# Kernel tuning notes

Measured on AMD Instinct MI355X. Metric: run time of the kernel, lower is better.

## Reference

```python
import jax, jax.numpy as jnp
import numpy as np

WD, WH, WW = 2, 7, 7          # window size (D, H, W)
SD, SH, SW = 1, 3, 3          # shift size
DIM, NH = 128, 4              # channels, heads
B, D, H, W = 8, 8, 56, 56     # input dims
N = WD * WH * WW              # tokens per window = 98
HIDDEN = int(DIM * 4.0)


def _rel_index_np():
    coords = np.stack(np.meshgrid(np.arange(WD), np.arange(WH), np.arange(WW), indexing='ij'))
    coords = coords.reshape(3, -1)                      # [3, N]
    rel = (coords[:, :, None] - coords[:, None, :]).transpose(1, 2, 0)  # [N, N, 3]
    rel[:, :, 0] += WD - 1
    rel[:, :, 1] += WH - 1
    rel[:, :, 2] += WW - 1
    rel[:, :, 0] *= (2 * WH - 1) * (2 * WW - 1)
    rel[:, :, 1] *= (2 * WW - 1)
    return rel.sum(-1).astype(np.int32)                 # [N, N]


def _window_partition_np(x):
    b, d, h, w, c = x.shape
    x = x.reshape(b, d // WD, WD, h // WH, WH, w // WW, WW, c)
    return x.transpose(0, 1, 3, 5, 2, 4, 6, 7).reshape(-1, N, c)


def _attn_mask_np():
    img = np.zeros((1, D, H, W, 1), np.float32)
    cnt = 0
    for ds in (slice(0, -WD), slice(-WD, -SD), slice(-SD, None)):
        for hs in (slice(0, -WH), slice(-WH, -SH), slice(-SH, None)):
            for ws in (slice(0, -WW), slice(-WW, -SW), slice(-SW, None)):
                img[:, ds, hs, ws, :] = cnt
                cnt += 1
    mw = _window_partition_np(img).reshape(-1, N)       # [nW, N]
    am = mw[:, None, :] - mw[:, :, None]
    return np.where(am != 0, -100.0, 0.0).astype(np.float32)  # [nW, N, N]


def setup_inputs() -> dict:
    key = jax.random.key(0)
    ks = jax.random.split(key, 8)
    s = 0.02
    return {
        'x': jax.random.normal(ks[0], (B, D, H, W, DIM), jnp.float32),
        'mask_matrix': jnp.asarray(_attn_mask_np()),
        'rel_index': jnp.asarray(_rel_index_np()),
        'norm1_g': jnp.ones((DIM,), jnp.float32),
        'norm1_b': jnp.zeros((DIM,), jnp.float32),
        'qkv_w': s * jax.random.normal(ks[1], (DIM, 3 * DIM), jnp.float32),
        'qkv_b': jnp.zeros((3 * DIM,), jnp.float32),
        'rpb': s * jax.random.normal(ks[2], ((2 * WD - 1) * (2 * WH - 1) * (2 * WW - 1), NH), jnp.float32),
        'proj_w': s * jax.random.normal(ks[3], (DIM, DIM), jnp.float32),
        'proj_b': jnp.zeros((DIM,), jnp.float32),
        'norm2_g': jnp.ones((DIM,), jnp.float32),
        'norm2_b': jnp.zeros((DIM,), jnp.float32),
        'fc1_w': s * jax.random.normal(ks[4], (DIM, HIDDEN), jnp.float32),
        'fc1_b': jnp.zeros((HIDDEN,), jnp.float32),
        'fc2_w': s * jax.random.normal(ks[5], (HIDDEN, DIM), jnp.float32),
        'fc2_b': jnp.zeros((DIM,), jnp.float32),
    }


def _ln(x, g, b):
    mu = jnp.mean(x, -1, keepdims=True)
    v = jnp.mean((x - mu) ** 2, -1, keepdims=True)
    return (x - mu) * jax.lax.rsqrt(v + 1e-5) * g + b


def _partition(x):
    b, d, h, w, c = x.shape
    x = x.reshape(b, d // WD, WD, h // WH, WH, w // WW, WW, c)
    return x.transpose(0, 1, 3, 5, 2, 4, 6, 7).reshape(-1, N, c)


def _reverse(win, b, d, h, w):
    c = win.shape[-1]
    x = win.reshape(b, d // WD, h // WH, w // WW, WD, WH, WW, c)
    return x.transpose(0, 1, 4, 2, 5, 3, 6, 7).reshape(b, d, h, w, c)


def _forward(x, mask_matrix, rel_index, norm1_g, norm1_b, qkv_w, qkv_b, rpb,
             proj_w, proj_b, norm2_g, norm2_b, fc1_w, fc1_b, fc2_w, fc2_b):
    b, d, h, w, c = x.shape
    shortcut = x
    y = _ln(x, norm1_g, norm1_b)
    # pad to multiples of window size (static; 0 for chosen dims)
    pd, ph, pw = (-d) % WD, (-h) % WH, (-w) % WW
    y = jnp.pad(y, ((0, 0), (0, pd), (0, ph), (0, pw), (0, 0)))
    dp, hp, wp = d + pd, h + ph, w + pw
    # cyclic shift
    y = jnp.roll(y, (-SD, -SH, -SW), axis=(1, 2, 3))
    win = _partition(y)                                   # [Bw, N, C]
    bw = win.shape[0]
    hd = c // NH
    qkv = (win @ qkv_w + qkv_b).reshape(bw, N, 3, NH, hd).transpose(2, 0, 3, 1, 4)
    q, k, v = qkv[0] * (hd ** -0.5), qkv[1], qkv[2]       # [Bw, NH, N, hd]
    attn = jnp.einsum('bhnd,bhmd->bhnm', q, k)            # [Bw, NH, N, N]
    bias = rpb[rel_index].transpose(2, 0, 1)              # [NH, N, N]
    attn = attn + bias[None]
    nw = mask_matrix.shape[0]
    attn = attn.reshape(bw // nw, nw, NH, N, N) + mask_matrix[None, :, None]
    attn = jax.nn.softmax(attn.reshape(bw, NH, N, N), axis=-1)
    o = jnp.einsum('bhnm,bhmd->bhnd', attn, v).transpose(0, 2, 1, 3).reshape(bw, N, c)
    o = o @ proj_w + proj_b
    y = _reverse(o, b, dp, hp, wp)
    y = jnp.roll(y, (SD, SH, SW), axis=(1, 2, 3))[:, :d, :h, :w, :]
    x1 = shortcut + y                                     # first residual
    z = _ln(x1, norm2_g, norm2_b)
    z = jax.nn.gelu(z @ fc1_w + fc1_b, approximate=False)
    # NOTE: source code's call() returns drop_path(mlp(norm2(x))) WITHOUT the
    # second residual add; we replicate exactly (drop_path is Identity at rate 0).
    return z @ fc2_w + fc2_b


def reference(x, mask_matrix, rel_index, norm1_g, norm1_b, qkv_w, qkv_b, rpb,
              proj_w, proj_b, norm2_g, norm2_b, fc1_w, fc1_b, fc2_w, fc2_b):
    return _forward(x, mask_matrix, rel_index, norm1_g, norm1_b, qkv_w, qkv_b,
                    rpb, proj_w, proj_b, norm2_g, norm2_b, fc1_w, fc1_b, fc2_w, fc2_b)


if __name__ == '__main__':
    out = reference(**setup_inputs())
    print(out.shape)
```

## Files before the change

### kernel.cpp

```cpp
#include <hip/hip_runtime.h>
#include <hip/hip_bf16.h>

typedef __attribute__((ext_vector_type(8))) short bf16x8;
typedef __attribute__((ext_vector_type(4))) float f32x4;

#define MFMA(a,b,c) __builtin_amdgcn_mfma_f32_16x16x32_bf16((a),(b),(c),0,0,0)
#define WAVE_LDS_FENCE() do { asm volatile("s_waitcnt lgkmcnt(0)" ::: "memory"); \
                              __builtin_amdgcn_sched_barrier(0); } while (0)

static constexpr int NTOK = 8 * 8 * 56 * 56;
static constexpr int NT   = 98;
static constexpr int NWIN = 2048;
static constexpr int NN   = NT * NT;

__device__ __forceinline__ unsigned short f2bf(float f) {
  unsigned r;
  asm("v_cvt_pk_bf16_f32 %0, %1, %1" : "=v"(r) : "v"(f));
  return (unsigned short)r;
}
__device__ __forceinline__ unsigned f2bf2(float lo, float hi) {
  unsigned r;
  asm("v_cvt_pk_bf16_f32 %0, %1, %2" : "=v"(r) : "v"(lo), "v"(hi));
  return r;
}
__device__ __forceinline__ float bf2f(unsigned short s) {
  union { unsigned u; float f; } v; v.u = ((unsigned)s) << 16; return v.f;
}
union U8 { unsigned u[4]; bf16x8 v; };

__device__ __forceinline__ size_t srow_of(int t) {
  int widx = t / NT, n = t - widx * NT;
  int bb = widx >> 8, wb = widx & 255;
  int dW = wb >> 6, hW = (wb >> 3) & 7, wW = wb & 7;
  int dr = n / 49, rem = n - dr * 49, hr = rem / 7, wr = rem - hr * 7;
  int dsh = (dW * 2 + dr + 1) & 7;
  int hs = hW * 7 + hr + 3; if (hs >= 56) hs -= 56;
  int wsv = wW * 7 + wr + 3; if (wsv >= 56) wsv -= 56;
  return ((size_t)(bb * 8 + dsh) * 56 + hs) * 56 + wsv;
}

__global__ __launch_bounds__(256) void k0_prep(
    const float* __restrict__ qkv_w, const float* __restrict__ proj_w,
    const float* __restrict__ fc1_w, const float* __restrict__ fc2_w,
    const float* __restrict__ n1g, const float* __restrict__ n1b,
    const float* __restrict__ qkv_b,
    unsigned short* __restrict__ qkvT, unsigned short* __restrict__ projT,
    unsigned short* __restrict__ fc1T, unsigned short* __restrict__ fc2T,
    float* __restrict__ qbb) {
  int idx = blockIdx.x * 256 + threadIdx.x;
  if (idx < 384 * 128) {
    int n = idx >> 7, k = idx & 127;
    float sc = n < 128 ? 0.17677669529663687f : 1.0f;
    qkvT[idx] = f2bf(qkv_w[k * 384 + n] * n1g[k] * sc);
  }
  if (idx < 128 * 128) { int n = idx >> 7, k = idx & 127; projT[idx] = f2bf(proj_w[k * 128 + n]); }
  if (idx < 512 * 128) { int n = idx >> 7, k = idx & 127; fc1T[idx] = f2bf(fc1_w[k * 512 + n]); }
  if (idx < 128 * 512) { int n = idx >> 9, k = idx & 511; fc2T[idx] = f2bf(fc2_w[k * 128 + n]); }
  if (idx < 384) {
    float acc = qkv_b[idx];
    for (int k = 0; k < 128; ++k) acc += n1b[k] * qkv_w[k * 384 + idx];
    qbb[idx] = acc * (idx < 128 ? 0.17677669529663687f : 1.0f);
  }
}

__global__ __launch_bounds__(256) void k0b_cmb(
    const int* __restrict__ rel, const float* __restrict__ rpb,
    const float* __restrict__ mask, unsigned short* __restrict__ cmb) {
  int idx = blockIdx.x * 256 + threadIdx.x;
  if (idx >= 4 * 8 * 98 * 128) return;
  int nt = idx & 7;
  int l15 = (idx >> 3) & 15;
  int rest = idx >> 7;
  int i = rest % 98;
  int hc = rest / 98;
  int h = hc >> 3, cls = hc & 7;
  int col = nt * 16 + l15;
  float val = 0.f;
  if (nt < 7 && col < 98) {
    int wb_rep = ((cls >> 2) & 1 ? 192 : 0) + ((cls >> 1) & 1 ? 56 : 0) + ((cls & 1) ? 7 : 0);
    val = rpb[rel[i * NT + col] * 4 + h] + mask[(size_t)wb_rep * NN + i * NT + col];
  }
  cmb[idx] = f2bf(val);
}

__global__ __launch_bounds__(256, 2) void k2_qkv(
    const float* __restrict__ x, const unsigned short* __restrict__ qkvT,
    const float* __restrict__ qbb,
    unsigned short* __restrict__ q, unsigned short* __restrict__ k,
    unsigned short* __restrict__ v) {
  __shared__ __align__(16) unsigned short wsW[64 * 136];
  int tid = threadIdx.x, wv = tid >> 6, lane = tid & 63;
  int l15 = lane & 15, lhi = lane >> 4;
  int mbase = blockIdx.x * 128 + wv * 32;

  bf16x8 afr[2][4];
#pragma unroll
  for (int mt = 0; mt < 2; ++mt) {
    int row = mbase + mt * 16 + l15;
    size_t srow = srow_of(row);
    const float* xr = x + srow * 128 + lhi * 8;
    float xv[4][8];
    float s = 0.f, ss = 0.f;
#pragma unroll
    for (int ks = 0; ks < 4; ++ks) {
      float4 lo = *(const float4*)(xr + ks * 32);
      float4 hi = *(const float4*)(xr + ks * 32 + 4);
      xv[ks][0] = lo.x; xv[ks][1] = lo.y; xv[ks][2] = lo.z; xv[ks][3] = lo.w;
      xv[ks][4] = hi.x; xv[ks][5] = hi.y; xv[ks][6] = hi.z; xv[ks][7] = hi.w;
#pragma unroll
      for (int e = 0; e < 8; ++e) { s += xv[ks][e]; ss += xv[ks][e] * xv[ks][e]; }
    }
    s += __shfl_xor(s, 16);  ss += __shfl_xor(ss, 16);
    s += __shfl_xor(s, 32);  ss += __shfl_xor(ss, 32);
    float mu = s * (1.f / 128.f);
    float var = ss * (1.f / 128.f) - mu * mu;
    float inv = __builtin_amdgcn_rsqf(var + 1e-5f);
#pragma unroll
    for (int ks = 0; ks < 4; ++ks) {
      U8 t;
#pragma unroll
      for (int p = 0; p < 4; ++p)
        t.u[p] = f2bf2((xv[ks][2 * p] - mu) * inv, (xv[ks][2 * p + 1] - mu) * inv);
      afr[mt][ks] = t.v;
    }
  }

  int rbase[2][4];
#pragma unroll
  for (int mt = 0; mt < 2; ++mt)
#pragma unroll
    for (int j = 0; j < 4; ++j) {
      int r = mbase + mt * 16 + lhi * 4 + j;
      int widx = r / NT, n = r - widx * NT;
      rbase[mt][j] = widx * 392 + n;
    }

  bf16x8 pf[4];
#pragma unroll
  for (int u = 0; u < 4; ++u) pf[u] = *(const bf16x8*)(qkvT + u * 2048 + tid * 8);

  for (int ch = 0; ch < 6; ++ch) {
#pragma unroll
    for (int u = 0; u < 4; ++u) {
      int flat = u * 2048 + tid * 8;
      *(bf16x8*)(&wsW[(flat >> 7) * 136 + (flat & 127)]) = pf[u];
    }
    __syncthreads();
    if (ch < 5) {
#pragma unroll
      for (int u = 0; u < 4; ++u)
        pf[u] = *(const bf16x8*)(qkvT + (ch + 1) * 8192 + u * 2048 + tid * 8);
    }
    f32x4 acc[2][4] = {};
#pragma unroll
    for (int ks = 0; ks < 4; ++ks)
#pragma unroll
      for (int nt = 0; nt < 4; ++nt) {
        bf16x8 bfr = *(const bf16x8*)(&wsW[(nt * 16 + l15) * 136 + ks * 32 + lhi * 8]);
#pragma unroll
        for (int mt = 0; mt < 2; ++mt)
          acc[mt][nt] = MFMA(afr[mt][ks], bfr, acc[mt][nt]);
      }
#pragma unroll
    for (int nt = 0; nt < 4; ++nt) {
      int col = ch * 64 + nt * 16 + l15;
      int which = col >> 7, head = (col >> 5) & 3, hd = col & 31;
      unsigned short* outb = which == 0 ? q : (which == 1 ? k : v);
      float bias = qbb[col];
#pragma unroll
      for (int mt = 0; mt < 2; ++mt)
#pragma unroll
        for (int j = 0; j < 4; ++j) {
          float val = acc[mt][nt][j] + bias;
          outb[(size_t)(rbase[mt][j] + head * 98) * 32 + hd] = f2bf(val);
        }
    }
    __syncthreads();
  }
}

__global__ __launch_bounds__(512) void k3_attn(
    const unsigned short* __restrict__ q, const unsigned short* __restrict__ kk,
    const unsigned short* __restrict__ vv, const unsigned short* __restrict__ cmb,
    unsigned short* __restrict__ out) {
  __shared__ __align__(16) unsigned short Vt[32 * 140];
  __shared__ __align__(16) unsigned short Pw[7][16 * 140];
  int bid = blockIdx.x;
  int widx = bid >> 2, head = bid & 3;
  int wb = widx & 255;
  size_t base = (size_t)(widx * 4 + head) * NT * 32;
  int tid = threadIdx.x, wv = tid >> 6, lane = tid & 63;
  int l15 = lane & 15, lhi = lane >> 4;

  for (int idx = tid; idx < NT * 32; idx += 512) {
    int j = idx >> 5, d = idx & 31;
    Vt[d * 140 + j] = vv[base + idx];
  }
  for (int idx = tid; idx < 32 * 30; idx += 512) {
    int d = idx / 30, j = 98 + idx % 30;
    Vt[d * 140 + j] = 0;
  }
  __syncthreads();
  if (wv >= 7) return;

  int cls = (((wb >> 6) == 3) << 2) | ((((wb >> 3) & 7) == 7) << 1) | ((int)((wb & 7) == 7));
  const unsigned short* cw = cmb + (size_t)(head * 8 + cls) * 98 * 128;
  unsigned short* P = Pw[wv];
  int mb = wv * 16;

  bf16x8 afr = *(const bf16x8*)(q + base + (size_t)(mb + l15) * 32 + lhi * 8);
  f32x4 sfr[7];
#pragma unroll
  for (int nt = 0; nt < 7; ++nt) {
    bf16x8 bfr = *(const bf16x8*)(kk + base + (size_t)(nt * 16 + l15) * 32 + lhi * 8);
    f32x4 zz = {};
    sfr[nt] = MFMA(afr, bfr, zz);
  }
#pragma unroll
  for (int j = 0; j < 4; ++j) {
    int i = mb + lhi * 4 + j;
    int ic = i < 97 ? i : 97;
    bf16x8 cv = *(const bf16x8*)(cw + ic * 128 + l15 * 8);
    float sv[7];
#pragma unroll
    for (int nt = 0; nt < 7; ++nt) {
      int colc = nt * 16 + l15;
      float s = fminf(fmaxf(sfr[nt][j], -1e4f), 1e4f);
      float bm = bf2f((unsigned short)cv[nt]);
      sv[nt] = (i < NT && colc < NT) ? (s + bm) : -1e30f;
    }
    float mx = sv[0];
#pragma unroll
    for (int nt = 1; nt < 7; ++nt) mx = fmaxf(mx, sv[nt]);
#pragma unroll
    for (int m2 = 1; m2 < 16; m2 <<= 1) mx = fmaxf(mx, __shfl_xor(mx, m2));
    float sum = 0.f, p[7];
#pragma unroll
    for (int nt = 0; nt < 7; ++nt) { p[nt] = __expf(sv[nt] - mx); sum += p[nt]; }
#pragma unroll
    for (int m2 = 1; m2 < 16; m2 <<= 1) sum += __shfl_xor(sum, m2);
    float inv = __builtin_amdgcn_rcpf(sum);
    int iloc = lhi * 4 + j;
#pragma unroll
    for (int nt = 0; nt < 7; ++nt)
      P[iloc * 140 + nt * 16 + l15] = f2bf(p[nt] * inv);
    P[iloc * 140 + 112 + l15] = 0;
  }
  WAVE_LDS_FENCE();

  f32x4 ofr[2] = {};
#pragma unroll
  for (int ks = 0; ks < 4; ++ks) {
    bf16x8 pafr = *(const bf16x8*)(P + l15 * 140 + ks * 32 + lhi * 8);
#pragma unroll
    for (int nt = 0; nt < 2; ++nt) {
      bf16x8 bfr = *(const bf16x8*)(Vt + (nt * 16 + l15) * 140 + ks * 32 + lhi * 8);
      ofr[nt] = MFMA(pafr, bfr, ofr[nt]);
    }
  }
#pragma unroll
  for (int nt = 0; nt < 2; ++nt)
#pragma unroll
    for (int j = 0; j < 4; ++j) {
      int n = mb + lhi * 4 + j;
      if (n < NT) {
        int d = nt * 16 + l15;
        out[(size_t)(widx * NT + n) * 128 + head * 32 + d] = f2bf(ofr[nt][j]);
      }
    }
}

__global__ __launch_bounds__(256, 3) void k4_proj_ln(
    const unsigned short* __restrict__ ao, const unsigned short* __restrict__ projT,
    const float* __restrict__ proj_b, const float* __restrict__ x,
    const float* __restrict__ g2, const float* __restrict__ b2,
    unsigned short* __restrict__ z) {
  __shared__ __align__(16) unsigned short wsW[128 * 136];
  int tid = threadIdx.x, wv = tid >> 6, lane = tid & 63;
  int l15 = lane & 15, lhi = lane >> 4;
  int mbase = blockIdx.x * 128 + wv * 32;
  int rl = lane >> 2, c0 = (lane & 3) * 32;

  size_t srows[2];
  srows[0] = srow_of(mbase + rl);
  srows[1] = srow_of(mbase + 16 + rl);
  float4 x0[8];
#pragma unroll
  for (int i = 0; i < 8; ++i)
    x0[i] = *(const float4*)(x + srows[0] * 128 + c0 + 4 * i);

#pragma unroll
  for (int u = 0; u < 8; ++u) {
    int flat = u * 2048 + tid * 8;
    *(bf16x8*)(&wsW[(flat >> 7) * 136 + (flat & 127)]) = *(const bf16x8*)(projT + flat);
  }
  bf16x8 afr[2][4];
#pragma unroll
  for (int mt = 0; mt < 2; ++mt)
#pragma unroll
    for (int ks = 0; ks < 4; ++ks)
      afr[mt][ks] = *(const bf16x8*)(ao + (size_t)(mbase + mt * 16 + l15) * 128 + ks * 32 + lhi * 8);
  __syncthreads();

  f32x4 acc[2][8] = {};
#pragma unroll
  for (int ks = 0; ks < 4; ++ks)
#pragma unroll
    for (int nt = 0; nt < 8; ++nt) {
      bf16x8 bfr = *(const bf16x8*)(&wsW[(nt * 16 + l15) * 136 + ks * 32 + lhi * 8]);
#pragma unroll
      for (int mt = 0; mt < 2; ++mt)
        acc[mt][nt] = MFMA(afr[mt][ks], bfr, acc[mt][nt]);
    }
  __syncthreads();

  float4 x1[8];
#pragma unroll
  for (int i = 0; i < 8; ++i)
    x1[i] = *(const float4*)(x + srows[1] * 128 + c0 + 4 * i);

  float* bounce = (float*)wsW + wv * (16 * 132);
  float pb[8];
#pragma unroll
  for (int nt = 0; nt < 8; ++nt) pb[nt] = proj_b[nt * 16 + l15];

#pragma unroll
  for (int mt = 0; mt < 2; ++mt) {
#pragma unroll
    for (int nt = 0; nt < 8; ++nt)
#pragma unroll
      for (int j = 0; j < 4; ++j)
        bounce[(lhi * 4 + j) * 132 + nt * 16 + l15] = acc[mt][nt][j] + pb[nt];
    WAVE_LDS_FENCE();

    size_t srow = srows[mt];
    float vals[32];
    float s = 0.f, ss = 0.f;
#pragma unroll
    for (int i = 0; i < 8; ++i) {
      float4 pv = *(const float4*)(bounce + rl * 132 + c0 + 4 * i);
      float4 xv = mt == 0 ? x0[i] : x1[i];
      float a0 = pv.x + xv.x, a1 = pv.y + xv.y, a2 = pv.z + xv.z, a3 = pv.w + xv.w;
      vals[4 * i] = a0; vals[4 * i + 1] = a1; vals[4 * i + 2] = a2; vals[4 * i + 3] = a3;
      s += a0 + a1 + a2 + a3;
      ss += a0 * a0 + a1 * a1 + a2 * a2 + a3 * a3;
    }
    s += __shfl_xor(s, 1);  ss += __shfl_xor(ss, 1);
    s += __shfl_xor(s, 2);  ss += __shfl_xor(ss, 2);
    float mu = s * (1.f / 128.f);
    float var = ss * (1.f / 128.f) - mu * mu;
    float inv = __builtin_amdgcn_rsqf(var + 1e-5f);
    unsigned pk[16];
#pragma unroll
    for (int i = 0; i < 8; ++i) {
      float4 g = *(const float4*)(g2 + c0 + 4 * i);
      float4 b = *(const float4*)(b2 + c0 + 4 * i);
      pk[2 * i]     = f2bf2((vals[4 * i]     - mu) * inv * g.x + b.x,
                            (vals[4 * i + 1] - mu) * inv * g.y + b.y);
      pk[2 * i + 1] = f2bf2((vals[4 * i + 2] - mu) * inv * g.z + b.z,
                            (vals[4 * i + 3] - mu) * inv * g.w + b.w);
    }
    unsigned* zp = (unsigned*)(z + srow * 128 + c0);
#pragma unroll
    for (int i = 0; i < 4; ++i)
      *(uint4*)(zp + 4 * i) = make_uint4(pk[4 * i], pk[4 * i + 1], pk[4 * i + 2], pk[4 * i + 3]);
    WAVE_LDS_FENCE();
  }
}

__global__ __launch_bounds__(256, 2) void k5_mlp(
    const unsigned short* __restrict__ z, const unsigned short* __restrict__ fc1T,
    const float* __restrict__ fc1_b, const unsigned short* __restrict__ fc2T,
    const float* __restrict__ fc2_b, float* __restrict__ out) {
  __shared__ __align__(16) unsigned short wsA[64 * 132];
  __shared__ __align__(16) unsigned short wsB[128 * 68];
  __shared__ __align__(16) unsigned short hl[4][32 * 70];
  int tid = threadIdx.x, wv = tid >> 6, lane = tid & 63;
  int l15 = lane & 15, lhi = lane >> 4;
  int mbase = blockIdx.x * 128 + wv * 32;
  unsigned short* hw = hl[wv];

  bf16x8 afr[2][4];
#pragma unroll
  for (int mt = 0; mt < 2; ++mt)
#pragma unroll
    for (int ks = 0; ks < 4; ++ks)
      afr[mt][ks] = *(const bf16x8*)(z + (size_t)(mbase + mt * 16 + l15) * 128 + ks * 32 + lhi * 8);

  bf16x8 pfA[4], pfB[4];
#pragma unroll
  for (int u = 0; u < 4; ++u) pfA[u] = *(const bf16x8*)(fc1T + u * 2048 + tid * 8);
#pragma unroll
  for (int u = 0; u < 4; ++u) {
    int flat = u * 2048 + tid * 8;
    pfB[u] = *(const bf16x8*)(fc2T + (size_t)(flat >> 6) * 512 + (flat & 63));
  }

  f32x4 oacc[2][8] = {};
  for (int ch = 0; ch < 8; ++ch) {
#pragma unroll
    for (int u = 0; u < 4; ++u) {
      int flat = u * 2048 + tid * 8;
      *(bf16x8*)(&wsA[(flat >> 7) * 132 + (flat & 127)]) = pfA[u];
      *(bf16x8*)(&wsB[(flat >> 6) * 68 + (flat & 63)]) = pfB[u];
    }
    __syncthreads();
    if (ch < 7) {
#pragma unroll
      for (int u = 0; u < 4; ++u)
        pfA[u] = *(const bf16x8*)(fc1T + (ch + 1) * 8192 + u * 2048 + tid * 8);
#pragma unroll
      for (int u = 0; u < 4; ++u) {
        int flat = u * 2048 + tid * 8;
        pfB[u] = *(const bf16x8*)(fc2T + (size_t)(flat >> 6) * 512 + (ch + 1) * 64 + (flat & 63));
      }
    }
    f32x4 hacc[2][4] = {};
#pragma unroll
    for (int ks = 0; ks < 4; ++ks)
#pragma unroll
      for (int nt = 0; nt < 4; ++nt) {
        bf16x8 bfr = *(const bf16x8*)(&wsA[(nt * 16 + l15) * 132 + ks * 32 + lhi * 8]);
#pragma unroll
        for (int mt = 0; mt < 2; ++mt)
          hacc[mt][nt] = MFMA(afr[mt][ks], bfr, hacc[mt][nt]);
      }
#pragma unroll
    for (int mt = 0; mt < 2; ++mt)
#pragma unroll
      for (int nt = 0; nt < 4; ++nt)
#pragma unroll
        for (int j = 0; j < 4; ++j) {
          int r = mt * 16 + lhi * 4 + j;
          int hcol = ch * 64 + nt * 16 + l15;
          float hv = hacc[mt][nt][j] + fc1_b[hcol];
          float targ = hv * (1.5957691216f + 0.0713548162f * hv * hv);
          float gv = hv * __builtin_amdgcn_rcpf(1.0f + __expf(-targ));
          hw[r * 70 + nt * 16 + l15] = f2bf(gv);
        }
    WAVE_LDS_FENCE();
#pragma unroll
    for (int ks = 0; ks < 2; ++ks) {
      bf16x8 a2[2];
#pragma unroll
      for (int mt = 0; mt < 2; ++mt)
        a2[mt] = *(const bf16x8*)(&hw[(mt * 16 + l15) * 70 + ks * 32 + lhi * 8]);
#pragma unroll
      for (int nt = 0; nt < 8; ++nt) {
        bf16x8 bfr = *(const bf16x8*)(&wsB[(nt * 16 + l15) * 68 + ks * 32 + lhi * 8]);
#pragma unroll
        for (int mt = 0; mt < 2; ++mt)
          oacc[mt][nt] = MFMA(a2[mt], bfr, oacc[mt][nt]);
      }
    }
    WAVE_LDS_FENCE();
    __syncthreads();
  }
#pragma unroll
  for (int mt = 0; mt < 2; ++mt)
#pragma unroll
    for (int nt = 0; nt < 8; ++nt)
#pragma unroll
      for (int j = 0; j < 4; ++j) {
        int r = mbase + mt * 16 + lhi * 4 + j;
        out[(size_t)r * 128 + nt * 16 + l15] = oacc[mt][nt][j] + fc2_b[nt * 16 + l15];
      }
}

extern "C" void kernel_launch(void* const* d_in, const int* in_sizes, int n_in,
                              void* d_out, int out_size, void* d_ws, size_t ws_size,
                              hipStream_t stream) {
  const float* x      = (const float*)d_in[0];
  const float* mask   = (const float*)d_in[1];
  const int*   rel    = (const int*)d_in[2];
  const float* n1g    = (const float*)d_in[3];
  const float* n1b    = (const float*)d_in[4];
  const float* qkv_w  = (const float*)d_in[5];
  const float* qkv_b  = (const float*)d_in[6];
  const float* rpb    = (const float*)d_in[7];
  const float* proj_w = (const float*)d_in[8];
  const float* proj_b = (const float*)d_in[9];
  const float* n2g    = (const float*)d_in[10];
  const float* n2b    = (const float*)d_in[11];
  const float* fc1_w  = (const float*)d_in[12];
  const float* fc1_b  = (const float*)d_in[13];
  const float* fc2_w  = (const float*)d_in[14];
  const float* fc2_b  = (const float*)d_in[15];
  float* out = (float*)d_out;

  char* ws = (char*)d_ws;
  const size_t SZ = (size_t)NTOK * 128 * 2;
  unsigned short* win   = (unsigned short*)(ws);
  unsigned short* qb    = (unsigned short*)(ws + SZ);
  unsigned short* kb    = (unsigned short*)(ws + 2 * SZ);
  unsigned short* vb    = (unsigned short*)(ws + 3 * SZ);
  unsigned short* qkvT  = (unsigned short*)(ws + 4 * SZ);
  unsigned short* projT = qkvT + 384 * 128;
  unsigned short* fc1T  = projT + 128 * 128;
  unsigned short* fc2T  = fc1T + 512 * 128;
  unsigned short* cmb   = fc2T + 128 * 512;
  float* qbb            = (float*)(cmb + (size_t)4 * 8 * 98 * 128);
  unsigned short* ao = win;
  unsigned short* zb = qb;

  k0_prep<<<256, 256, 0, stream>>>(qkv_w, proj_w, fc1_w, fc2_w, n1g, n1b, qkv_b,
                                   qkvT, projT, fc1T, fc2T, qbb);
  k0b_cmb<<<(4 * 8 * 98 * 128 + 255) / 256, 256, 0, stream>>>(rel, rpb, mask, cmb);
  k2_qkv<<<NTOK / 128, 256, 0, stream>>>(x, qkvT, qbb, qb, kb, vb);
  k3_attn<<<NWIN * 4, 512, 0, stream>>>(qb, kb, vb, cmb, ao);
  k4_proj_ln<<<NTOK / 128, 256, 0, stream>>>(ao, projT, proj_b, x, n2g, n2b, zb);
  k5_mlp<<<NTOK / 128, 256, 0, stream>>>(zb, fc1T, fc1_b, fc2T, fc2_b, out);
}
```

Before: 352.8 us.

## Relax LDS fences, hoist bias loads, and interleave GELU with fc2 MFMAs

Removes the sched_barrier from the wave-level LDS fence so the compiler can schedule instructions across it. In the attention kernel it hoists the combined bias/mask loads ahead of the QK MFMAs and drops the score clamp. In the MLP kernel it splits GELU into two halves, each followed by its K-slice of fc2 MFMAs, so activation math can overlap matrix work. Without the sched_barrier the compiler may reorder LDS accesses in unintended ways, and dropping the clamp changes behaviour for extreme scores.

Result: no change. 356.6 us (median of 2 runs) (+1.1%).

```diff
diff --git a/kernel.cpp b/kernel.cpp
--- a/kernel.cpp
+++ b/kernel.cpp
@@ -5,8 +5,7 @@
 typedef __attribute__((ext_vector_type(4))) float f32x4;
 
 #define MFMA(a,b,c) __builtin_amdgcn_mfma_f32_16x16x32_bf16((a),(b),(c),0,0,0)
-#define WAVE_LDS_FENCE() do { asm volatile("s_waitcnt lgkmcnt(0)" ::: "memory"); \
-                              __builtin_amdgcn_sched_barrier(0); } while (0)
+#define WAVE_SYNC() asm volatile("s_waitcnt lgkmcnt(0)" ::: "memory")
 
 static constexpr int NTOK = 8 * 8 * 56 * 56;
 static constexpr int NT   = 98;
@@ -208,6 +207,14 @@
   unsigned short* P = Pw[wv];
   int mb = wv * 16;
 
+  bf16x8 cv[4];
+#pragma unroll
+  for (int j = 0; j < 4; ++j) {
+    int i = mb + lhi * 4 + j;
+    int ic = i < 97 ? i : 97;
+    cv[j] = *(const bf16x8*)(cw + ic * 128 + l15 * 8);
+  }
+
   bf16x8 afr = *(const bf16x8*)(q + base + (size_t)(mb + l15) * 32 + lhi * 8);
   f32x4 sfr[7];
 #pragma unroll
@@ -219,15 +226,12 @@
 #pragma unroll
   for (int j = 0; j < 4; ++j) {
     int i = mb + lhi * 4 + j;
-    int ic = i < 97 ? i : 97;
-    bf16x8 cv = *(const bf16x8*)(cw + ic * 128 + l15 * 8);
     float sv[7];
 #pragma unroll
     for (int nt = 0; nt < 7; ++nt) {
       int colc = nt * 16 + l15;
-      float s = fminf(fmaxf(sfr[nt][j], -1e4f), 1e4f);
-      float bm = bf2f((unsigned short)cv[nt]);
-      sv[nt] = (i < NT && colc < NT) ? (s + bm) : -1e30f;
+      float bm = bf2f((unsigned short)cv[j][nt]);
+      sv[nt] = (i < NT && colc < NT) ? (sfr[nt][j] + bm) : -1e30f;
     }
     float mx = sv[0];
 #pragma unroll
@@ -246,7 +250,7 @@
       P[iloc * 140 + nt * 16 + l15] = f2bf(p[nt] * inv);
     P[iloc * 140 + 112 + l15] = 0;
   }
-  WAVE_LDS_FENCE();
+  WAVE_SYNC();
 
   f32x4 ofr[2] = {};
 #pragma unroll
@@ -331,7 +335,7 @@
 #pragma unroll
       for (int j = 0; j < 4; ++j)
         bounce[(lhi * 4 + j) * 132 + nt * 16 + l15] = acc[mt][nt][j] + pb[nt];
-    WAVE_LDS_FENCE();
+    WAVE_SYNC();
 
     size_t srow = srows[mt];
     float vals[32];
@@ -364,7 +368,7 @@
 #pragma unroll
     for (int i = 0; i < 4; ++i)
       *(uint4*)(zp + 4 * i) = make_uint4(pk[4 * i], pk[4 * i + 1], pk[4 * i + 2], pk[4 * i + 3]);
-    WAVE_LDS_FENCE();
+    WAVE_SYNC();
   }
 }
 
@@ -426,34 +430,36 @@
           hacc[mt][nt] = MFMA(afr[mt][ks], bfr, hacc[mt][nt]);
       }
 #pragma unroll
-    for (int mt = 0; mt < 2; ++mt)
-#pragma unroll
-      for (int nt = 0; nt < 4; ++nt)
-#pragma unroll
-        for (int j = 0; j < 4; ++j) {
-          int r = mt * 16 + lhi * 4 + j;
-          int hcol = ch * 64 + nt * 16 + l15;
-          float hv = hacc[mt][nt][j] + fc1_b[hcol];
-          float targ = hv * (1.5957691216f + 0.0713548162f * hv * hv);
-          float gv = hv * __builtin_amdgcn_rcpf(1.0f + __expf(-targ));
-          hw[r * 70 + nt * 16 + l15] = f2bf(gv);
+    for (int half = 0; half < 2; ++half) {
+#pragma unroll
+      for (int mt = 0; mt < 2; ++mt)
+#pragma unroll
+        for (int nt2 = 0; nt2 < 2; ++nt2) {
+          int nt = half * 2 + nt2;
+#pragma unroll
+          for (int j = 0; j < 4; ++j) {
+            int r = mt * 16 + lhi * 4 + j;
+            int hcol = ch * 64 + nt * 16 + l15;
+            float hv = hacc[mt][nt][j] + fc1_b[hcol];
+            float targ = hv * (1.5957691216f + 0.0713548162f * hv * hv);
+            float gv = hv * __builtin_amdgcn_rcpf(1.0f + __expf(-targ));
+            hw[r * 70 + nt * 16 + l15] = f2bf(gv);
+          }
         }
-    WAVE_LDS_FENCE();
-#pragma unroll
-    for (int ks = 0; ks < 2; ++ks) {
+      WAVE_SYNC();
       bf16x8 a2[2];
 #pragma unroll
       for (int mt = 0; mt < 2; ++mt)
-        a2[mt] = *(const bf16x8*)(&hw[(mt * 16 + l15) * 70 + ks * 32 + lhi * 8]);
+        a2[mt] = *(const bf16x8*)(&hw[(mt * 16 + l15) * 70 + half * 32 + lhi * 8]);
 #pragma unroll
       for (int nt = 0; nt < 8; ++nt) {
-        bf16x8 bfr = *(const bf16x8*)(&wsB[(nt * 16 + l15) * 68 + ks * 32 + lhi * 8]);
+        bf16x8 bfr = *(const bf16x8*)(&wsB[(nt * 16 + l15) * 68 + half * 32 + lhi * 8]);
 #pragma unroll
         for (int mt = 0; mt < 2; ++mt)
           oacc[mt][nt] = MFMA(a2[mt], bfr, oacc[mt][nt]);
       }
     }
-    WAVE_LDS_FENCE();
+    WAVE_SYNC();
     __syncthreads();
   }
 #pragma unroll
```
